# Kernel tuning notes

Hardware: AMD Instinct MI355X
Metric: run time of the kernel (lower is better)

The kernel has to match this reference:

```python
import jax, jax.numpy as jnp
import numpy as np

B, P, T, R, A = 16384, 3, 2, 3, 3   # batch, n_players, teammates, rivals, action_dim
HID = [1024, 512]
ENC_OUT = 64
RIVAL_START = 9 * 9 + 12 * P       # 117, as in the torch module
NEG_SLOPE = 0.01                    # nn.LeakyReLU default


def _linpack(key, k, din, dout):
    # PyTorch nn.Linear default init: U(-1/sqrt(din), 1/sqrt(din))
    kw, kb = jax.random.split(key)
    bound = 1.0 / np.sqrt(din)
    W = jax.random.uniform(kw, (k, din, dout), jnp.float32, -bound, bound)
    b = jax.random.uniform(kb, (k, dout), jnp.float32, -bound, bound)
    return W, b


def setup_inputs() -> dict:
    key = jax.random.key(0)
    ks = jax.random.split(key, 16)
    obs = jax.random.normal(ks[0], (B, P, 144), jnp.float32)
    act = jax.random.normal(ks[1], (B, P, A), jnp.float32)
    # stacked per-segment encoder weights (grouped small GEMMs)
    Wp1, bp1 = _linpack(ks[2], 9, 2 + A, 32)
    Wp2, bp2 = _linpack(ks[3], 9, 32, ENC_OUT)
    Wt1, bt1 = _linpack(ks[4], T, 12, 32)
    Wt2, bt2 = _linpack(ks[5], T, 32, ENC_OUT)
    Wr1, br1 = _linpack(ks[6], R, 9, 32)
    Wr2, br2 = _linpack(ks[7], R, 32, ENC_OUT)
    # q head: [P*896] -> 1024 -> 512 -> P
    din = P * (9 + T + R) * ENC_OUT
    Wq1, bq1 = _linpack(ks[8], 1, din, HID[0]);  Wq1, bq1 = Wq1[0], bq1[0]
    Wq2, bq2 = _linpack(ks[9], 1, HID[0], HID[1]); Wq2, bq2 = Wq2[0], bq2[0]
    Wq3, bq3 = _linpack(ks[10], 1, HID[1], P);   Wq3, bq3 = Wq3[0], bq3[0]
    return dict(obs=obs, act=act,
                Wp1=Wp1, bp1=bp1, Wp2=Wp2, bp2=bp2,
                Wt1=Wt1, bt1=bt1, Wt2=Wt2, bt2=bt2,
                Wr1=Wr1, br1=br1, Wr2=Wr2, br2=br2,
                Wq1=Wq1, bq1=bq1, Wq2=Wq2, bq2=bq2, Wq3=Wq3, bq3=bq3)


def _enc2(x, W1, b1, W2, b2):
    # x: [B, P, K, din]; W1: [K, din, 32]; W2: [K, 32, 64] -> [B, P, K, 64]
    lrelu = lambda v: jax.nn.leaky_relu(v, NEG_SLOPE)
    h = lrelu(jnp.einsum('bpki,kio->bpko', x, W1) + b1)
    return lrelu(jnp.einsum('bpkh,kho->bpko', h, W2) + b2)


def reference(obs, act, Wp1, bp1, Wp2, bp2, Wt1, bt1, Wt2, bt2,
              Wr1, br1, Wr2, br2, Wq1, bq1, Wq2, bq2, Wq3, bq3):
    b = obs.shape[0]
    # prop segments: obs[:, :, 2i:2i+2] concat act  -> [B, P, 9, 2+A]
    x_prop = jnp.concatenate(
        [obs[:, :, :18].reshape(b, P, 9, 2),
         jnp.broadcast_to(act[:, :, None, :], (b, P, 9, A))], axis=-1)
    x_team = obs[:, :, 18:18 + 12 * T].reshape(b, P, T, 12)
    x_riv = obs[:, :, RIVAL_START:RIVAL_START + 9 * R].reshape(b, P, R, 9)
    ep = _enc2(x_prop, Wp1, bp1, Wp2, bp2)   # [B, P, 9, 64]
    et = _enc2(x_team, Wt1, bt1, Wt2, bt2)   # [B, P, T, 64]
    er = _enc2(x_riv, Wr1, br1, Wr2, br2)    # [B, P, R, 64]
    enc = jnp.concatenate([ep, et, er], axis=2).reshape(b, -1)  # [B, P*14*64]
    # q head: ReLU hidden activations, identity output
    h = jax.nn.relu(enc @ Wq1 + bq1)
    h = jax.nn.relu(h @ Wq2 + bq2)
    return h @ Wq3 + bq3                      # [B, P]
```

## Files before the change

### kernel.cpp

```cpp
#include <hip/hip_runtime.h>
#include <hip/hip_bf16.h>
#include <cstdint>

typedef __bf16 bf16x8 __attribute__((ext_vector_type(8)));
typedef float f32x4 __attribute__((ext_vector_type(4)));

__device__ __forceinline__ void gld16(const __bf16* g, __bf16* lds) {
    __builtin_amdgcn_global_load_lds(
        (__attribute__((address_space(1))) void*)(uintptr_t)g,
        (__attribute__((address_space(3))) void*)(uint32_t)(uintptr_t)lds,
        16, 0, 0);
}

__global__ __launch_bounds__(256) void prep_all(const float* __restrict__ Wq1, const float* __restrict__ Wq2,
                                                const float* __restrict__ Wp1, const float* __restrict__ bp1,
                                                const float* __restrict__ Wp2, const float* __restrict__ bp2,
                                                const float* __restrict__ Wt1, const float* __restrict__ bt1,
                                                const float* __restrict__ Wt2, const float* __restrict__ bt2,
                                                const float* __restrict__ Wr1, const float* __restrict__ br1,
                                                const float* __restrict__ Wr2, const float* __restrict__ br2,
                                                __bf16* __restrict__ w1t, __bf16* __restrict__ w2t,
                                                float* __restrict__ w1p, __bf16* __restrict__ w2e) {
    __shared__ float t[64][65];
    const int idx = blockIdx.x, tid = threadIdx.x;
    if (idx < 800) {
        const float* in; __bf16* out; int R, C, bx, by;
        if (idx < 672) { in = Wq1; out = w1t; R = 2688; C = 1024; bx = idx % 42; by = idx / 42; }
        else { const int i2 = idx - 672; in = Wq2; out = w2t; R = 1024; C = 512; bx = i2 % 16; by = i2 / 16; }
        const int r0 = bx * 64, c0 = by * 64;
#pragma unroll
        for (int i = 0; i < 16; i++) {
            int id2 = i * 256 + tid;
            int rr = id2 >> 6, cc = id2 & 63;
            t[rr][cc] = in[(size_t)(r0 + rr) * C + (c0 + cc)];
        }
        __syncthreads();
#pragma unroll
        for (int i = 0; i < 16; i++) {
            int id2 = i * 256 + tid;
            int rr = id2 >> 6, cc = id2 & 63;
            out[(size_t)(c0 + rr) * R + (r0 + cc)] = (__bf16)t[cc][rr];
        }
    } else {
        const int s = idx - 800;
        int ks, din, w1off;
        const float *W1, *B1, *W2, *B2;
        if (s < 9)      { ks = s;      din = 5;  w1off = s * 160;
                          W1 = Wp1; B1 = bp1; W2 = Wp2; B2 = bp2; }
        else if (s < 11){ ks = s - 9;  din = 12; w1off = 1440 + ks * 384;
                          W1 = Wt1; B1 = bt1; W2 = Wt2; B2 = bt2; }
        else            { ks = s - 11; din = 9;  w1off = 2208 + ks * 288;
                          W1 = Wr1; B1 = br1; W2 = Wr2; B2 = br2; }
        W1 += ks * din * 32; B1 += ks * 32; W2 += ks * 2048; B2 += ks * 64;
        for (int i = tid; i < din * 32; i += 256) w1p[w1off + i] = W1[i];
        if (tid < 32) w1p[3072 + s * 32 + tid] = B1[tid];
        if (tid < 64) w1p[3520 + s * 64 + tid] = B2[tid];
        for (int i = tid; i < 2048; i += 256) {
            const int o = i >> 5, k = i & 31;
            w2e[s * 2048 + i] = (__bf16)W2[k * 64 + o];
        }
    }
}

__global__ __launch_bounds__(256) void enc_fused(const float* __restrict__ obs,
                                                 const float* __restrict__ act,
                                                 const float* __restrict__ w1p,
                                                 const __bf16* __restrict__ w2t,
                                                 __bf16* __restrict__ enc) {
    __shared__ float sW[4416];
    __shared__ __bf16 sH[2][64 * 40];
    __shared__ __align__(16) __bf16 sO[2][64 * 72];
    const int tid = threadIdx.x;
    for (int i = tid; i < 4416; i += 256) sW[i] = w1p[i];
    const int rloc = tid >> 2, q = tid & 3;
    const int row = blockIdx.x * 64 + rloc;
    const float* orow = obs + (size_t)row * 144;
    const float a0 = act[row * 3], a1 = act[row * 3 + 1], a2 = act[row * 3 + 2];
    const int wv = tid >> 6, lane = tid & 63;
    const int fr = lane & 15, kq = lane >> 4;

    bf16x8 bfrA[4], bfrB[4];
    int curH = 0, curO = 0;

    auto prefetchB = [&](int sn) {
#pragma unroll
        for (int n = 0; n < 4; n++)
            bfrB[n] = *(const bf16x8*)&w2t[(sn * 64 + n * 16 + fr) * 32 + kq * 8];
    };
    auto storeOut = [&](int sp, int bO) {
#pragma unroll
        for (int h = 0; h < 2; h++) {
            const int c = tid + h * 256;
            const int r = c >> 3, ch = c & 7;
            const bf16x8 v = *(const bf16x8*)&sO[bO][r * 72 + ch * 8];
            *(bf16x8*)&enc[((size_t)blockIdx.x * 64 + r) * 896 + sp * 64 + ch * 8] = v;
        }
    };
    auto l2c = [&](int s, int bH, int bO) {
        const bf16x8 afr = *(const bf16x8*)&sH[bH][(wv * 16 + fr) * 40 + kq * 8];
        f32x4 acc[4] = {};
#pragma unroll
        for (int n = 0; n < 4; n++)
            acc[n] = __builtin_amdgcn_mfma_f32_16x16x32_bf16(afr, bfrA[n], acc[n], 0, 0, 0);
        const float* b2 = sW + 3520 + s * 64;
#pragma unroll
        for (int n = 0; n < 4; n++) {
            const float bv = b2[n * 16 + fr];
#pragma unroll
            for (int rg = 0; rg < 4; rg++) {
                float v = acc[n][rg] + bv;
                v = fmaxf(v, 0.01f * v);
                sO[bO][(wv * 16 + kq * 4 + rg) * 72 + n * 16 + fr] = (__bf16)v;
            }
        }
    };

#define L1(DIN, W1OFF, SGI, DH, XLOAD)                               \
    {                                                                \
        float x[DIN];                                                \
        XLOAD;                                                       \
        const float* w1 = sW + (W1OFF);                              \
        const float* b1 = sW + 3072 + (SGI) * 32;                    \
        bf16x8 t_;                                                   \
        _Pragma("unroll") for (int j = 0; j < 8; j++) {              \
            const int o = q * 8 + j;                                 \
            float a_ = b1[o];                                        \
            _Pragma("unroll") for (int i = 0; i < DIN; i++)          \
                a_ += x[i] * w1[i * 32 + o];                         \
            t_[j] = (__bf16)fmaxf(a_, 0.01f * a_);                   \
        }                                                            \
        *(bf16x8*)&sH[DH][rloc * 40 + q * 8] = t_;                   \
    }

#define PROPX(K) { x[0] = orow[2 * (K)]; x[1] = orow[2 * (K) + 1]; x[2] = a0; x[3] = a1; x[4] = a2; }
#define TEAMX(K) { _Pragma("unroll") for (int i = 0; i < 12; i++) x[i] = orow[18 + 12 * (K) + i]; }
#define RIVX(K)  { _Pragma("unroll") for (int i = 0; i < 9; i++) x[i] = orow[117 + 9 * (K) + i]; }

#define STEP(S, NEXTL1)                                              \
    __syncthreads();                                                 \
    if ((S) < 13) prefetchB((S) + 1);                                \
    if ((S) > 0) storeOut((S) - 1, curO ^ 1);                        \
    l2c((S), curH, curO);                                            \
    _Pragma("unroll") for (int n = 0; n < 4; n++) bfrA[n] = bfrB[n]; \
    NEXTL1                                                           \
    curH ^= 1; curO ^= 1;

    prefetchB(0);
    __syncthreads();
#pragma unroll
    for (int n = 0; n < 4; n++) bfrA[n] = bfrB[n];
    L1(5, 0, 0, 0, PROPX(0))

    STEP(0,  L1(5, 160, 1, curH ^ 1, PROPX(1)))
    STEP(1,  L1(5, 320, 2, curH ^ 1, PROPX(2)))
    STEP(2,  L1(5, 480, 3, curH ^ 1, PROPX(3)))
    STEP(3,  L1(5, 640, 4, curH ^ 1, PROPX(4)))
    STEP(4,  L1(5, 800, 5, curH ^ 1, PROPX(5)))
    STEP(5,  L1(5, 960, 6, curH ^ 1, PROPX(6)))
    STEP(6,  L1(5, 1120, 7, curH ^ 1, PROPX(7)))
    STEP(7,  L1(5, 1280, 8, curH ^ 1, PROPX(8)))
    STEP(8,  L1(12, 1440, 9, curH ^ 1, TEAMX(0)))
    STEP(9,  L1(12, 1824, 10, curH ^ 1, TEAMX(1)))
    STEP(10, L1(9, 2208, 11, curH ^ 1, RIVX(0)))
    STEP(11, L1(9, 2496, 12, curH ^ 1, RIVX(1)))
    STEP(12, L1(9, 2784, 13, curH ^ 1, RIVX(2)))
    STEP(13, )

    __syncthreads();
    storeOut(13, curO ^ 1);
#undef STEP
#undef L1
#undef PROPX
#undef TEAMX
#undef RIVX
}

template <int NB>
__global__ __launch_bounds__(512, 2) void gemm256_relu(const __bf16* __restrict__ Ag,
                                                       const __bf16* __restrict__ Btg,
                                                       const float* __restrict__ bias,
                                                       __bf16* __restrict__ Cg,
                                                       int N, int K, int lgn) {
    __shared__ __align__(16) __bf16 ldsA[2][2][128 * 64];
    __shared__ __align__(16) __bf16 ldsB[2][2][NB * 64 * 64];
    const int tid = threadIdx.x;
    const int wid = tid >> 6, lane = tid & 63;
    const int wm = wid >> 2, wn = wid & 3;
    const int fr = lane & 15, kq = lane >> 4;

    const int chunk = gridDim.x >> 3;
    const int wg = (blockIdx.x & 7) * chunk + (blockIdx.x >> 3);
    const int bn = wg & ((1 << lgn) - 1), bm = wg >> lgn;

    const int c0 = tid, c1 = tid + 512;
    const int r0 = c0 >> 3, s0 = (c0 & 7) ^ (r0 & 7);
    const int r1 = c1 >> 3, s1 = (c1 & 7) ^ (r1 & 7);
    const size_t aH = (size_t)128 * K;
    const size_t bH = (size_t)(NB * 64) * K;
    const __bf16* aB0 = Ag + (size_t)(bm * 256 + r0) * K + s0 * 8;
    const __bf16* aB1 = Ag + (size_t)(bm * 256 + r1) * K + s1 * 8;
    const __bf16* bB0 = Btg + (size_t)(bn * (NB * 128) + r0) * K + s0 * 8;
    const __bf16* bB1 = Btg + (size_t)(bn * (NB * 128) + r1) * K + s1 * 8;

    f32x4 acc[2][2][4][NB] = {};
    bf16x8 a0[4][2], a1[4][2], b0[NB][2], b1[NB][2];

#define STAGE_A(BUF, H, KO)                                   \
    do {                                                      \
        __bf16* d_ = &ldsA[BUF][H][0];                        \
        gld16(aB0 + (H)*aH + (KO), d_ + c0 * 8);              \
        gld16(aB1 + (H)*aH + (KO), d_ + c1 * 8);              \
    } while (0)
#define STAGE_B(BUF, H, KO)                                   \
    do {                                                      \
        __bf16* d_ = &ldsB[BUF][H][0];                        \
        gld16(bB0 + (H)*bH + (KO), d_ + c0 * 8);              \
        if constexpr (NB == 2) gld16(bB1 + (H)*bH + (KO), d_ + c1 * 8); \
    } while (0)

#define LDFA(BUF, H, ROW, KS) \
    (*(const bf16x8*)&ldsA[BUF][H][(ROW) * 64 + ((((KS)*4 + kq) ^ ((ROW)&7)) * 8)])
#define LDFB(BUF, H, ROW, KS) \
    (*(const bf16x8*)&ldsB[BUF][H][(ROW) * 64 + ((((KS)*4 + kq) ^ ((ROW)&7)) * 8)])

#define LOAD_A(BUF, H, DST)                                   \
    _Pragma("unroll") for (int m = 0; m < 4; m++)             \
        _Pragma("unroll") for (int ks = 0; ks < 2; ks++)      \
            DST[m][ks] = LDFA(BUF, H, wm * 64 + m * 16 + fr, ks);
#define LOAD_B(BUF, H, DST)                                   \
    _Pragma("unroll") for (int n = 0; n < NB; n++)            \
        _Pragma("unroll") for (int ks = 0; ks < 2; ks++)      \
            DST[n][ks] = LDFB(BUF, H, wn * (NB * 16) + n * 16 + fr, ks);

#define MM(Q, R, AR, BR)                                      \
    __builtin_amdgcn_s_setprio(1);                            \
    _Pragma("unroll") for (int ks = 0; ks < 2; ks++)          \
        _Pragma("unroll") for (int m = 0; m < 4; m++)         \
            _Pragma("unroll") for (int n = 0; n < NB; n++)    \
                acc[Q][R][m][n] = __builtin_amdgcn_mfma_f32_16x16x32_bf16( \
                    AR[m][ks], BR[n][ks], acc[Q][R][m][n], 0, 0, 0); \
    __builtin_amdgcn_s_setprio(0);

#define SB0 __builtin_amdgcn_sched_barrier(0)
#define BAR __builtin_amdgcn_s_barrier()
#define LGKM_B1                                               \
    if constexpr (NB == 2) asm volatile("s_waitcnt lgkmcnt(4)" ::: "memory"); \
    else asm volatile("s_waitcnt lgkmcnt(2)" ::: "memory");
#define LGKM(NSTR) asm volatile("s_waitcnt lgkmcnt(" NSTR ")" ::: "memory")
#define VMW(NSTR) asm volatile("s_waitcnt vmcnt(" NSTR ")" ::: "memory")
#define VMW2(N2, N1)                                          \
    if constexpr (NB == 2) VMW(#N2); else VMW(#N1);

    const int NT = K >> 6;

    STAGE_A(0, 0, 0);
    STAGE_B(0, 0, 0);
    STAGE_B(0, 1, 0);
    STAGE_A(0, 1, 0);
    VMW("2");
    BAR;
    LOAD_A(0, 0, a0)
    LOAD_B(0, 0, b0)
    SB0;

    for (int t = 0; t < NT - 1; ++t) {
        const int buf = t & 1, nb = buf ^ 1;
        const int kO = (t + 1) << 6;

        STAGE_A(nb, 0, kO);
        STAGE_B(nb, 0, kO);
        VMW2(4, 3);
        LOAD_B(buf, 1, b1)
        SB0;
        BAR;
        LGKM_B1;
        SB0;
        MM(0, 0, a0, b0)

        STAGE_B(nb, 1, kO);
        STAGE_A(nb, 1, kO);
        LOAD_A(buf, 1, a1)
        SB0;
        BAR;
        LGKM("8");
        SB0;
        MM(0, 1, a0, b1)

        BAR;
        LGKM("0");
        SB0;
        MM(1, 0, a1, b0)

        VMW("2");
        BAR;
        LOAD_A(nb, 0, a0)
        LOAD_B(nb, 0, b0)
        SB0;
        MM(1, 1, a1, b1)
    }

    {
        const int buf = (NT - 1) & 1;
        VMW("0");
        LOAD_B(buf, 1, b1)
        SB0;
        BAR;
        LGKM_B1;
        SB0;
        MM(0, 0, a0, b0)

        LOAD_A(buf, 1, a1)
        SB0;
        BAR;
        LGKM("8");
        SB0;
        MM(0, 1, a0, b1)

        BAR;
        LGKM("0");
        SB0;
        MM(1, 0, a1, b0)

        MM(1, 1, a1, b1)
    }

    const int cc = lane & 15, rr = (lane >> 4) << 2;
#pragma unroll
    for (int q = 0; q < 2; q++)
#pragma unroll
        for (int r2 = 0; r2 < 2; r2++)
#pragma unroll
            for (int m = 0; m < 4; m++)
#pragma unroll
                for (int n = 0; n < NB; n++) {
                    const int colG = bn * (NB * 128) + r2 * (NB * 64) + wn * (NB * 16) + n * 16 + cc;
                    const int rowG = bm * 256 + q * 128 + wm * 64 + m * 16 + rr;
                    const float bv = bias[colG];
#pragma unroll
                    for (int reg = 0; reg < 4; reg++) {
                        float v = acc[q][r2][m][n][reg] + bv;
                        v = fmaxf(v, 0.0f);
                        Cg[(size_t)(rowG + reg) * N + colG] = (__bf16)v;
                    }
                }
#undef STAGE_A
#undef STAGE_B
#undef LDFA
#undef LDFB
#undef LOAD_A
#undef LOAD_B
#undef MM
#undef SB0
#undef BAR
#undef LGKM_B1
#undef LGKM
#undef VMW
#undef VMW2
}

__global__ __launch_bounds__(256) void head_kernel(const __bf16* __restrict__ h2,
                                                   const float* __restrict__ Wq3,
                                                   const float* __restrict__ bq3,
                                                   float* __restrict__ out) {
    const int wave = threadIdx.x >> 6, lane = threadIdx.x & 63;
    const int row = blockIdx.x * 4 + wave;
    const bf16x8 hv = *(const bf16x8*)(h2 + (size_t)row * 512 + lane * 8);
    float s0 = 0.f, s1 = 0.f, s2 = 0.f;
#pragma unroll
    for (int i = 0; i < 8; i++) {
        const float hf = (float)hv[i];
        const int k = lane * 8 + i;
        s0 += hf * Wq3[k * 3 + 0];
        s1 += hf * Wq3[k * 3 + 1];
        s2 += hf * Wq3[k * 3 + 2];
    }
#pragma unroll
    for (int off = 32; off > 0; off >>= 1) {
        s0 += __shfl_xor(s0, off);
        s1 += __shfl_xor(s1, off);
        s2 += __shfl_xor(s2, off);
    }
    if (lane == 0) {
        float* o = out + (size_t)row * 3;
        o[0] = s0 + bq3[0];
        o[1] = s1 + bq3[1];
        o[2] = s2 + bq3[2];
    }
}

extern "C" void kernel_launch(void* const* d_in, const int* in_sizes, int n_in,
                              void* d_out, int out_size, void* d_ws, size_t ws_size,
                              hipStream_t stream) {
    const float* obs = (const float*)d_in[0];
    const float* act = (const float*)d_in[1];
    const float* Wp1 = (const float*)d_in[2];  const float* bp1 = (const float*)d_in[3];
    const float* Wp2 = (const float*)d_in[4];  const float* bp2 = (const float*)d_in[5];
    const float* Wt1 = (const float*)d_in[6];  const float* bt1 = (const float*)d_in[7];
    const float* Wt2 = (const float*)d_in[8];  const float* bt2 = (const float*)d_in[9];
    const float* Wr1 = (const float*)d_in[10]; const float* br1 = (const float*)d_in[11];
    const float* Wr2 = (const float*)d_in[12]; const float* br2 = (const float*)d_in[13];
    const float* Wq1 = (const float*)d_in[14]; const float* bq1 = (const float*)d_in[15];
    const float* Wq2 = (const float*)d_in[16]; const float* bq2 = (const float*)d_in[17];
    const float* Wq3 = (const float*)d_in[18]; const float* bq3 = (const float*)d_in[19];
    float* out = (float*)d_out;

    char* ws = (char*)d_ws;
    __bf16* enc = (__bf16*)(ws);
    __bf16* h1  = (__bf16*)(ws + 88080384);
    __bf16* h2  = (__bf16*)(ws + 88080384 + 33554432);
    __bf16* w1t = (__bf16*)(ws + 138412032);
    __bf16* w2t = (__bf16*)(ws + 143917056);
    float*  w1p = (float*)(ws + 144965632);
    __bf16* w2e = (__bf16*)(ws + 144983296);

    prep_all<<<814, 256, 0, stream>>>(Wq1, Wq2, Wp1, bp1, Wp2, bp2, Wt1, bt1, Wt2, bt2,
                                      Wr1, br1, Wr2, br2, w1t, w2t, w1p, w2e);

    enc_fused<<<768, 256, 0, stream>>>(obs, act, w1p, w2e, enc);

    gemm256_relu<2><<<dim3(256), 512, 0, stream>>>(enc, w1t, bq1, h1, 1024, 2688, 2);
    gemm256_relu<1><<<dim3(256), 512, 0, stream>>>(h1, w2t, bq2, h2, 512, 1024, 2);
    head_kernel<<<16384 / 4, 256, 0, stream>>>(h2, Wq3, bq3, out);
}
```

Measured before the change: 137.8 us.

## Fuse final 512->3 head projection into second GEMM epilogue with partial sums

The second hidden-layer GEMM no longer writes its 16384x512 bf16 activation to global memory. Each tile stages its ReLU output in swizzled LDS and computes partial dot products with Wq3 for its 128-column slice. A tiny reduce kernel then sums the four per-column-block partials and adds the bias. This drops a 16 MB write and re-read plus a launch, at the cost of a longer GEMM epilogue with an extra barrier and scalar Wq3 loads.

```diff
diff --git a/kernel.cpp b/kernel.cpp
--- a/kernel.cpp
+++ b/kernel.cpp
@@ -175,14 +175,15 @@
 #undef RIVX
 }
 
-template <int NB>
+template <int NB, bool HEAD>
 __global__ __launch_bounds__(512, 2) void gemm256_relu(const __bf16* __restrict__ Ag,
                                                        const __bf16* __restrict__ Btg,
                                                        const float* __restrict__ bias,
                                                        __bf16* __restrict__ Cg,
+                                                       const float* __restrict__ Wq3,
+                                                       float* __restrict__ pout,
                                                        int N, int K, int lgn) {
-    __shared__ __align__(16) __bf16 ldsA[2][2][128 * 64];
-    __shared__ __align__(16) __bf16 ldsB[2][2][NB * 64 * 64];
+    __shared__ __align__(16) __bf16 ldsF[32768 + 2 * 2 * NB * 4096];
     const int tid = threadIdx.x;
     const int wid = tid >> 6, lane = tid & 63;
     const int wm = wid >> 2, wn = wid & 3;
@@ -205,23 +206,26 @@
     f32x4 acc[2][2][4][NB] = {};
     bf16x8 a0[4][2], a1[4][2], b0[NB][2], b1[NB][2];
 
+#define LDSA(BUF, H) (ldsF + ((BUF) * 2 + (H)) * 8192)
+#define LDSB(BUF, H) (ldsF + 32768 + ((BUF) * 2 + (H)) * (NB * 4096))
+
 #define STAGE_A(BUF, H, KO)                                   \
     do {                                                      \
-        __bf16* d_ = &ldsA[BUF][H][0];                        \
+        __bf16* d_ = LDSA(BUF, H);                            \
         gld16(aB0 + (H)*aH + (KO), d_ + c0 * 8);              \
         gld16(aB1 + (H)*aH + (KO), d_ + c1 * 8);              \
     } while (0)
 #define STAGE_B(BUF, H, KO)                                   \
     do {                                                      \
-        __bf16* d_ = &ldsB[BUF][H][0];                        \
+        __bf16* d_ = LDSB(BUF, H);                            \
         gld16(bB0 + (H)*bH + (KO), d_ + c0 * 8);              \
         if constexpr (NB == 2) gld16(bB1 + (H)*bH + (KO), d_ + c1 * 8); \
     } while (0)
 
 #define LDFA(BUF, H, ROW, KS) \
-    (*(const bf16x8*)&ldsA[BUF][H][(ROW) * 64 + ((((KS)*4 + kq) ^ ((ROW)&7)) * 8)])
+    (*(const bf16x8*)&LDSA(BUF, H)[(ROW) * 64 + ((((KS)*4 + kq) ^ ((ROW)&7)) * 8)])
 #define LDFB(BUF, H, ROW, KS) \
-    (*(const bf16x8*)&ldsB[BUF][H][(ROW) * 64 + ((((KS)*4 + kq) ^ ((ROW)&7)) * 8)])
+    (*(const bf16x8*)&LDSB(BUF, H)[(ROW) * 64 + ((((KS)*4 + kq) ^ ((ROW)&7)) * 8)])
 
 #define LOAD_A(BUF, H, DST)                                   \
     _Pragma("unroll") for (int m = 0; m < 4; m++)             \
@@ -325,24 +329,73 @@
     }
 
     const int cc = lane & 15, rr = (lane >> 4) << 2;
-#pragma unroll
-    for (int q = 0; q < 2; q++)
-#pragma unroll
-        for (int r2 = 0; r2 < 2; r2++)
-#pragma unroll
-            for (int m = 0; m < 4; m++)
-#pragma unroll
-                for (int n = 0; n < NB; n++) {
-                    const int colG = bn * (NB * 128) + r2 * (NB * 64) + wn * (NB * 16) + n * 16 + cc;
-                    const int rowG = bm * 256 + q * 128 + wm * 64 + m * 16 + rr;
-                    const float bv = bias[colG];
+    if constexpr (!HEAD) {
+#pragma unroll
+        for (int q = 0; q < 2; q++)
+#pragma unroll
+            for (int r2 = 0; r2 < 2; r2++)
+#pragma unroll
+                for (int m = 0; m < 4; m++)
+#pragma unroll
+                    for (int n = 0; n < NB; n++) {
+                        const int colG = bn * (NB * 128) + r2 * (NB * 64) + wn * (NB * 16) + n * 16 + cc;
+                        const int rowG = bm * 256 + q * 128 + wm * 64 + m * 16 + rr;
+                        const float bv = bias[colG];
+#pragma unroll
+                        for (int reg = 0; reg < 4; reg++) {
+                            float v = acc[q][r2][m][n][reg] + bv;
+                            v = fmaxf(v, 0.0f);
+                            Cg[(size_t)(rowG + reg) * N + colG] = (__bf16)v;
+                        }
+                    }
+    } else {
+        __syncthreads();
+        __bf16* hS = ldsF;
+#pragma unroll
+        for (int q = 0; q < 2; q++)
+#pragma unroll
+            for (int r2 = 0; r2 < 2; r2++)
+#pragma unroll
+                for (int m = 0; m < 4; m++) {
+                    const int colL = r2 * 64 + wn * 16 + cc;
+                    const int rowL0 = q * 128 + wm * 64 + m * 16 + rr;
+                    const float bv = bias[bn * 128 + colL];
+                    const int slot = colL >> 3, pos = colL & 7;
 #pragma unroll
                     for (int reg = 0; reg < 4; reg++) {
-                        float v = acc[q][r2][m][n][reg] + bv;
+                        const int rowL = rowL0 + reg;
+                        float v = acc[q][r2][m][0][reg] + bv;
                         v = fmaxf(v, 0.0f);
-                        Cg[(size_t)(rowG + reg) * N + colG] = (__bf16)v;
+                        hS[rowL * 128 + (slot ^ (rowL & 7)) * 8 + pos] = (__bf16)v;
                     }
                 }
+        __syncthreads();
+        const int rowL = tid >> 1, half = tid & 1;
+        float s0 = 0.f, s1 = 0.f, s2 = 0.f;
+#pragma unroll
+        for (int c8 = 0; c8 < 8; c8++) {
+            const int lslot = half * 8 + c8;
+            const int pslot = half * 8 + (c8 ^ (rowL & 7));
+            const bf16x8 hv = *(const bf16x8*)&hS[rowL * 128 + pslot * 8];
+#pragma unroll
+            for (int j = 0; j < 8; j++) {
+                const float hf = (float)hv[j];
+                const int col = bn * 128 + lslot * 8 + j;
+                s0 += hf * Wq3[col * 3 + 0];
+                s1 += hf * Wq3[col * 3 + 1];
+                s2 += hf * Wq3[col * 3 + 2];
+            }
+        }
+        s0 += __shfl_xor(s0, 1);
+        s1 += __shfl_xor(s1, 1);
+        s2 += __shfl_xor(s2, 1);
+        if (!half) {
+            float* p = pout + ((size_t)(bm * 256 + rowL) * 4 + bn) * 3;
+            p[0] = s0; p[1] = s1; p[2] = s2;
+        }
+    }
+#undef LDSA
+#undef LDSB
 #undef STAGE_A
 #undef STAGE_B
 #undef LDFA
@@ -358,34 +411,14 @@
 #undef VMW2
 }
 
-__global__ __launch_bounds__(256) void head_kernel(const __bf16* __restrict__ h2,
-                                                   const float* __restrict__ Wq3,
+__global__ __launch_bounds__(256) void reduce_head(const float* __restrict__ pout,
                                                    const float* __restrict__ bq3,
                                                    float* __restrict__ out) {
-    const int wave = threadIdx.x >> 6, lane = threadIdx.x & 63;
-    const int row = blockIdx.x * 4 + wave;
-    const bf16x8 hv = *(const bf16x8*)(h2 + (size_t)row * 512 + lane * 8);
-    float s0 = 0.f, s1 = 0.f, s2 = 0.f;
-#pragma unroll
-    for (int i = 0; i < 8; i++) {
-        const float hf = (float)hv[i];
-        const int k = lane * 8 + i;
-        s0 += hf * Wq3[k * 3 + 0];
-        s1 += hf * Wq3[k * 3 + 1];
-        s2 += hf * Wq3[k * 3 + 2];
-    }
-#pragma unroll
-    for (int off = 32; off > 0; off >>= 1) {
-        s0 += __shfl_xor(s0, off);
-        s1 += __shfl_xor(s1, off);
-        s2 += __shfl_xor(s2, off);
-    }
-    if (lane == 0) {
-        float* o = out + (size_t)row * 3;
-        o[0] = s0 + bq3[0];
-        o[1] = s1 + bq3[1];
-        o[2] = s2 + bq3[2];
-    }
+    const int row = blockIdx.x * 256 + threadIdx.x;
+    const float* p = pout + (size_t)row * 12;
+#pragma unroll
+    for (int j = 0; j < 3; j++)
+        out[(size_t)row * 3 + j] = p[j] + p[3 + j] + p[6 + j] + p[9 + j] + bq3[j];
 }
 
 extern "C" void kernel_launch(void* const* d_in, const int* in_sizes, int n_in,
@@ -405,20 +438,20 @@
     float* out = (float*)d_out;
 
     char* ws = (char*)d_ws;
-    __bf16* enc = (__bf16*)(ws);
-    __bf16* h1  = (__bf16*)(ws + 88080384);
-    __bf16* h2  = (__bf16*)(ws + 88080384 + 33554432);
-    __bf16* w1t = (__bf16*)(ws + 138412032);
-    __bf16* w2t = (__bf16*)(ws + 143917056);
-    float*  w1p = (float*)(ws + 144965632);
-    __bf16* w2e = (__bf16*)(ws + 144983296);
+    __bf16* enc  = (__bf16*)(ws);
+    __bf16* h1   = (__bf16*)(ws + 88080384);
+    float*  pout = (float*)(ws + 88080384 + 33554432);
+    __bf16* w1t  = (__bf16*)(ws + 138412032);
+    __bf16* w2t  = (__bf16*)(ws + 143917056);
+    float*  w1p  = (float*)(ws + 144965632);
+    __bf16* w2e  = (__bf16*)(ws + 144983296);
 
     prep_all<<<814, 256, 0, stream>>>(Wq1, Wq2, Wp1, bp1, Wp2, bp2, Wt1, bt1, Wt2, bt2,
                                       Wr1, br1, Wr2, br2, w1t, w2t, w1p, w2e);
 
     enc_fused<<<768, 256, 0, stream>>>(obs, act, w1p, w2e, enc);
 
-    gemm256_relu<2><<<dim3(256), 512, 0, stream>>>(enc, w1t, bq1, h1, 1024, 2688, 2);
-    gemm256_relu<1><<<dim3(256), 512, 0, stream>>>(h1, w2t, bq2, h2, 512, 1024, 2);
-    head_kernel<<<16384 / 4, 256, 0, stream>>>(h2, Wq3, bq3, out);
-}
+    gemm256_relu<2, false><<<dim3(256), 512, 0, stream>>>(enc, w1t, bq1, h1, nullptr, nullptr, 1024, 2688, 2);
+    gemm256_relu<1, true><<<dim3(256), 512, 0, stream>>>(h1, w2t, bq2, nullptr, Wq3, pout, 512, 1024, 2);
+    reduce_head<<<64, 256, 0, stream>>>(pout, bq3, out);
+}
```

Result: no change. 136.7 us (-0.8%).
